# Kernel tuning notes

Hardware: AMD Instinct MI355X
Metric: run time of the kernel (lower is better)

## Reference

```python
import jax, jax.numpy as jnp
import numpy as np

N_STYLE_TOKEN = 10
TOKEN_SIZE = 256   # num_units
NUM_HEADS = 8
D_K = TOKEN_SIZE // NUM_HEADS  # 32, key_dim of cross-attention
D_Q = 256                      # encoder_hidden (add_gst=True, add_positional_encoding=True)
MAX_SEQ_LEN = 2000


def sinusoid_table(n_pos, d):
    pos = np.arange(n_pos, dtype=np.float64)[:, None]
    i = np.arange(d, dtype=np.float64)[None, :]
    angle = pos / np.power(10000.0, 2.0 * (i // 2) / d)
    table = np.zeros((n_pos, d), dtype=np.float64)
    table[:, 0::2] = np.sin(angle[:, 0::2])
    table[:, 1::2] = np.cos(angle[:, 1::2])
    return jnp.asarray(table, dtype=jnp.float32)


def setup_inputs() -> dict:
    key = jax.random.key(0)
    k1, k2, k3, k4, k5, k6 = jax.random.split(key, 6)
    N, T = 64, 2000
    inputs = jax.random.normal(k1, (N, T, D_Q), dtype=jnp.float32)
    positional_indexes = jnp.sort(
        jax.random.randint(k2, (N, T), 0, T), axis=-1).astype(jnp.int64)
    embed = 0.5 * jax.random.normal(k3, (N_STYLE_TOKEN, D_K), dtype=jnp.float32)
    # nn.Linear(in, out, bias=False) weights stored as [out, in]
    Wq = jax.random.normal(k4, (TOKEN_SIZE, D_Q), dtype=jnp.float32) / np.sqrt(D_Q)
    Wk = jax.random.normal(k5, (TOKEN_SIZE, D_K), dtype=jnp.float32) / np.sqrt(D_K)
    Wv = jax.random.normal(k6, (TOKEN_SIZE, D_K), dtype=jnp.float32) / np.sqrt(D_K)
    pos_table = sinusoid_table(MAX_SEQ_LEN + 1, D_Q)  # non-trainable buffer
    return {"inputs": inputs, "positional_indexes": positional_indexes,
            "embed": embed, "Wq": Wq, "Wk": Wk, "Wv": Wv,
            "pos_table": pos_table}


def reference(inputs, positional_indexes, embed, Wq, Wk, Wv, pos_table):
    N, T, dq = inputs.shape
    H, ds = NUM_HEADS, TOKEN_SIZE // NUM_HEADS
    n_tok, d_k = embed.shape

    # per-utterance positional gather (the python for-loop, vectorized):
    # pos_enc_by_scale[i, t] = pos_table[positional_indexes[i, t]]
    pos_enc = pos_table[positional_indexes]            # [N, T, dq]
    x = inputs + pos_enc                               # add_positional_encoding=True

    keys = jnp.tanh(embed)                             # [n_tok, d_k]

    q = jnp.einsum('ntq,uq->ntu', x, Wq)               # [N, T, U]
    k = keys @ Wk.T                                    # [n_tok, U]
    v = keys @ Wv.T                                    # [n_tok, U]

    qh = q.reshape(N, T, H, ds)                        # split heads along units
    kh = k.reshape(n_tok, H, ds)
    vh = v.reshape(n_tok, H, ds)

    logits = jnp.einsum('nthd,khd->nhtk', qh, kh) / jnp.sqrt(
        jnp.asarray(d_k, dtype=qh.dtype))              # [N, H, T, n_tok]
    attn = jax.nn.softmax(logits, axis=-1)

    out = jnp.einsum('nhtk,khd->nthd', attn, vh).reshape(N, T, H * ds)
    # scores: [h,N,T,k] pieces concatenated on last dim, then transpose(1,2)
    scores = jnp.transpose(attn, (0, 1, 3, 2)).reshape(N, H * n_tok, T)
    return out, scores
```

## Files before the change

### kernel.cpp

```cpp
#include <hip/hip_runtime.h>

#define T_SEQ 2000
#define N_UTT 64
#define DQ 256
#define NTOK 10
#define NH 8
#define DS 32

typedef float f32x4 __attribute__((ext_vector_type(4)));
typedef short s16x8 __attribute__((ext_vector_type(8)));

__device__ __forceinline__ unsigned short f2bf(float f){
    unsigned int u = __float_as_uint(f);
    u += 0x7FFFu + ((u >> 16) & 1u);
    return (unsigned short)(u >> 16);
}
__device__ __forceinline__ float bf2f(unsigned short h){
    return __uint_as_float(((unsigned int)h) << 16);
}

__global__ __launch_bounds__(256) void prep_kernel(
    const float* __restrict__ embed, const float* __restrict__ Wq,
    const float* __restrict__ Wk, const float* __restrict__ Wv,
    unsigned short* __restrict__ WqB, float* __restrict__ khd, float* __restrict__ vhd)
{
    const int b = blockIdx.x, t = threadIdx.x;
    if (b < 256){
        const int i = b*256 + t;
        WqB[i] = f2bf(Wq[i]);
    } else {
        for (int tok = 0; tok < NTOK; ++tok){
            float ka = 0.f, va = 0.f;
            #pragma unroll
            for (int d = 0; d < DS; ++d){
                const float kd = tanhf(embed[tok*DS + d]);
                ka += kd * Wk[t*DS + d];
                va += kd * Wv[t*DS + d];
            }
            khd[tok*256 + t] = ka;
            vhd[tok*256 + t] = va;
        }
    }
}

#define XS_STRIDE 264
#define QS_STRIDE 260

__global__ __launch_bounds__(256, 3) void main_kernel(
    const float* __restrict__ inputs, const int* __restrict__ pidx,
    const float* __restrict__ pos_table, const unsigned short* __restrict__ WqB,
    const float* __restrict__ khd, const float* __restrict__ vhd,
    float* __restrict__ outp, float* __restrict__ scores)
{
    __shared__ unsigned short xs_hi[16*XS_STRIDE];
    __shared__ unsigned short xs_lo[16*XS_STRIDE];
    __shared__ float qs[16*QS_STRIDE];
    __shared__ float khL[NTOK*256];
    __shared__ float vhL[NTOK*256];

    const int tid = threadIdx.x;
    const int m0 = blockIdx.x * 16;
    const int n  = m0 / T_SEQ;
    const int t0 = m0 % T_SEQ;

    #pragma unroll
    for (int i = 0; i < NTOK; ++i){
        khL[i*256 + tid] = khd[i*256 + tid];
        vhL[i*256 + tid] = vhd[i*256 + tid];
    }

    {
        const int rsub = tid >> 6;
        const int c    = (tid & 63) * 4;
        #pragma unroll
        for (int p = 0; p < 4; ++p){
            const int r   = p*4 + rsub;
            const int row = m0 + r;
            const int idx = pidx[row];
            const float4 xi = *(const float4*)(inputs    + (size_t)row*DQ + c);
            const float4 pe = *(const float4*)(pos_table + (size_t)idx*DQ + c);
            float xv[4] = {xi.x+pe.x, xi.y+pe.y, xi.z+pe.z, xi.w+pe.w};
            unsigned short hs[4], ls[4];
            #pragma unroll
            for (int j = 0; j < 4; ++j){
                hs[j] = f2bf(xv[j]);
                ls[j] = f2bf(xv[j] - bf2f(hs[j]));
            }
            *(uint2*)&xs_hi[r*XS_STRIDE + c] =
                make_uint2(hs[0] | ((unsigned)hs[1] << 16), hs[2] | ((unsigned)hs[3] << 16));
            *(uint2*)&xs_lo[r*XS_STRIDE + c] =
                make_uint2(ls[0] | ((unsigned)ls[1] << 16), ls[2] | ((unsigned)ls[3] << 16));
        }
    }
    __syncthreads();

    {
        const int wave = tid >> 6;
        const int lane = tid & 63;
        const int lrow = lane & 15;
        const int quad = lane >> 4;
        const int u0w  = wave * 64;

        s16x8 ah[8], al[8];
        #pragma unroll
        for (int kt = 0; kt < 8; ++kt){
            ah[kt] = *(const s16x8*)&xs_hi[lrow*XS_STRIDE + kt*32 + quad*8];
            al[kt] = *(const s16x8*)&xs_lo[lrow*XS_STRIDE + kt*32 + quad*8];
        }
        f32x4 acc[4] = {};
        #pragma unroll
        for (int kt = 0; kt < 8; ++kt){
            s16x8 bfr[4];
            #pragma unroll
            for (int ct = 0; ct < 4; ++ct){
                const int u = u0w + ct*16 + lrow;
                bfr[ct] = *(const s16x8*)(WqB + u*256 + kt*32 + quad*8);
            }
            #pragma unroll
            for (int ct = 0; ct < 4; ++ct){
                acc[ct] = __builtin_amdgcn_mfma_f32_16x16x32_bf16(al[kt], bfr[ct], acc[ct], 0,0,0);
                acc[ct] = __builtin_amdgcn_mfma_f32_16x16x32_bf16(ah[kt], bfr[ct], acc[ct], 0,0,0);
            }
        }
        #pragma unroll
        for (int ct = 0; ct < 4; ++ct){
            #pragma unroll
            for (int reg = 0; reg < 4; ++reg){
                qs[(quad*4 + reg)*QS_STRIDE + u0w + ct*16 + lrow] = acc[ct][reg];
            }
        }
    }
    __syncthreads();

    if (tid < 128){
        const int r = tid & 15;
        const int h = tid >> 4;
        const int t = t0 + r;

        float q[32];
        #pragma unroll
        for (int d = 0; d < 32; d += 4){
            const float4 v4 = *(const float4*)&qs[r*QS_STRIDE + h*32 + d];
            q[d+0]=v4.x; q[d+1]=v4.y; q[d+2]=v4.z; q[d+3]=v4.w;
        }
        const float scale = 0.17677669529663687f;
        float logit[NTOK];
        float mx = -1e30f;
        #pragma unroll
        for (int k = 0; k < NTOK; ++k){
            const float* kp = &khL[k*256 + h*32];
            float a0=0.f,a1=0.f,a2=0.f,a3=0.f;
            #pragma unroll
            for (int d = 0; d < 32; d += 4){
                a0 += q[d+0]*kp[d+0];
                a1 += q[d+1]*kp[d+1];
                a2 += q[d+2]*kp[d+2];
                a3 += q[d+3]*kp[d+3];
            }
            logit[k] = ((a0+a1)+(a2+a3))*scale;
            mx = fmaxf(mx, logit[k]);
        }
        float p[NTOK], s = 0.f;
        #pragma unroll
        for (int k = 0; k < NTOK; ++k){ p[k] = __expf(logit[k]-mx); s += p[k]; }
        const float inv = 1.f/s;
        #pragma unroll
        for (int k = 0; k < NTOK; ++k){
            p[k] *= inv;
            scores[(n*(NH*NTOK) + h*NTOK + k)*T_SEQ + t] = p[k];
        }
        #pragma unroll
        for (int d = 0; d < 32; d += 4){
            float4 o = make_float4(0.f,0.f,0.f,0.f);
            #pragma unroll
            for (int k = 0; k < NTOK; ++k){
                const float4 vv = *(const float4*)&vhL[k*256 + h*32 + d];
                o.x += p[k]*vv.x; o.y += p[k]*vv.y; o.z += p[k]*vv.z; o.w += p[k]*vv.w;
            }
            *(float4*)(outp + (size_t)(m0 + r)*DQ + h*32 + d) = o;
        }
    }
}

extern "C" void kernel_launch(void* const* d_in, const int* in_sizes, int n_in,
                              void* d_out, int out_size, void* d_ws, size_t ws_size,
                              hipStream_t stream)
{
    const float* inputs    = (const float*)d_in[0];
    const int*   pidx      = (const int*)d_in[1];
    const float* embed     = (const float*)d_in[2];
    const float* Wq        = (const float*)d_in[3];
    const float* Wk        = (const float*)d_in[4];
    const float* Wv        = (const float*)d_in[5];
    const float* pos_table = (const float*)d_in[6];

    float* outp   = (float*)d_out;
    float* scores = outp + (size_t)N_UTT*T_SEQ*DQ;

    unsigned short* WqB = (unsigned short*)d_ws;
    float* khd = (float*)((char*)d_ws + 256*256*sizeof(unsigned short));
    float* vhd = khd + NTOK*256;

    prep_kernel<<<257, 256, 0, stream>>>(embed, Wq, Wk, Wv, WqB, khd, vhd);
    main_kernel<<<8000, 256, 0, stream>>>(inputs, pidx, pos_table, WqB, khd, vhd,
                                          outp, scores);
}
```

Before: 460.5 us.

## Fold Wq and key projection into one logit weight matrix

Precomputes a combined 80x256 weight (Wq_h^T * k_h, with the softmax scale folded in) so the main kernel computes logits straight from x with one GEMM instead of projecting to 256-wide q and then taking dot products. The combined weight is split into bf16 hi/lo parts and the product uses three MFMAs for near-fp32 accuracy. The main kernel now runs one wave per 32 rows and loads x directly into registers without staging through LDS. This cuts GEMM width from 256 to 80 columns, at the cost of extra hi/lo MFMAs, an extra prep launch, and uncoalesced per-lane global loads.

```diff
diff --git a/kernel.cpp b/kernel.cpp
--- a/kernel.cpp
+++ b/kernel.cpp
@@ -6,6 +6,8 @@
 #define NTOK 10
 #define NH 8
 #define DS 32
+#define NC 80
+#define LGS 84
 
 typedef float f32x4 __attribute__((ext_vector_type(4)));
 typedef short s16x8 __attribute__((ext_vector_type(8)));
@@ -19,165 +21,148 @@
     return __uint_as_float(((unsigned int)h) << 16);
 }
 
-__global__ __launch_bounds__(256) void prep_kernel(
-    const float* __restrict__ embed, const float* __restrict__ Wq,
-    const float* __restrict__ Wk, const float* __restrict__ Wv,
-    unsigned short* __restrict__ WqB, float* __restrict__ khd, float* __restrict__ vhd)
+__global__ __launch_bounds__(256) void prep_kv(
+    const float* __restrict__ embed, const float* __restrict__ Wk,
+    const float* __restrict__ Wv, float* __restrict__ khd, float* __restrict__ vhd)
 {
-    const int b = blockIdx.x, t = threadIdx.x;
-    if (b < 256){
-        const int i = b*256 + t;
-        WqB[i] = f2bf(Wq[i]);
-    } else {
-        for (int tok = 0; tok < NTOK; ++tok){
-            float ka = 0.f, va = 0.f;
-            #pragma unroll
-            for (int d = 0; d < DS; ++d){
-                const float kd = tanhf(embed[tok*DS + d]);
-                ka += kd * Wk[t*DS + d];
-                va += kd * Wv[t*DS + d];
-            }
-            khd[tok*256 + t] = ka;
-            vhd[tok*256 + t] = va;
+    __shared__ float th[NTOK*DS];
+    const int u = threadIdx.x;
+    for (int i = u; i < NTOK*DS; i += 256) th[i] = tanhf(embed[i]);
+    __syncthreads();
+    for (int tok = 0; tok < NTOK; ++tok){
+        float ka = 0.f, va = 0.f;
+        #pragma unroll
+        for (int d = 0; d < DS; ++d){
+            const float kd = th[tok*DS + d];
+            ka += kd * Wk[u*DS + d];
+            va += kd * Wv[u*DS + d];
         }
+        khd[tok*DQ + u] = ka;
+        vhd[tok*DQ + u] = va;
     }
 }
 
-#define XS_STRIDE 264
-#define QS_STRIDE 260
+__global__ __launch_bounds__(256) void prep_wl(
+    const float* __restrict__ Wq, const float* __restrict__ khd,
+    unsigned short* __restrict__ WlH, unsigned short* __restrict__ WlL)
+{
+    const int c = blockIdx.x;
+    const int q = threadIdx.x;
+    const int h = c / NTOK, tok = c - h*NTOK;
+    float s = 0.f;
+    #pragma unroll
+    for (int d = 0; d < DS; ++d)
+        s += Wq[(size_t)(h*DS + d)*DQ + q] * khd[tok*DQ + h*DS + d];
+    s *= 0.17677669529663687f;
+    const unsigned short hi = f2bf(s);
+    const unsigned short lo = f2bf(s - bf2f(hi));
+    WlH[c*DQ + q] = hi;
+    WlL[c*DQ + q] = lo;
+}
 
-__global__ __launch_bounds__(256, 3) void main_kernel(
+__global__ __launch_bounds__(64, 4) void main_kernel(
     const float* __restrict__ inputs, const int* __restrict__ pidx,
-    const float* __restrict__ pos_table, const unsigned short* __restrict__ WqB,
-    const float* __restrict__ khd, const float* __restrict__ vhd,
+    const float* __restrict__ pos_table, const unsigned short* __restrict__ WlH,
+    const unsigned short* __restrict__ WlL, const float* __restrict__ vhd,
     float* __restrict__ outp, float* __restrict__ scores)
 {
-    __shared__ unsigned short xs_hi[16*XS_STRIDE];
-    __shared__ unsigned short xs_lo[16*XS_STRIDE];
-    __shared__ float qs[16*QS_STRIDE];
-    __shared__ float khL[NTOK*256];
-    __shared__ float vhL[NTOK*256];
+    __shared__ float lg[2][16][LGS];
+    const int lane = threadIdx.x;
+    const int lrow = lane & 15;
+    const int quad = lane >> 4;
+    const int m0   = blockIdx.x * 32;
 
-    const int tid = threadIdx.x;
-    const int m0 = blockIdx.x * 16;
-    const int n  = m0 / T_SEQ;
-    const int t0 = m0 % T_SEQ;
+    const int rowA = m0 + lrow;
+    const int rowB = rowA + 16;
+    const int idxA = pidx[rowA];
+    const int idxB = pidx[rowB];
 
-    #pragma unroll
-    for (int i = 0; i < NTOK; ++i){
-        khL[i*256 + tid] = khd[i*256 + tid];
-        vhL[i*256 + tid] = vhd[i*256 + tid];
-    }
+    f32x4 acc[2][5] = {};
 
-    {
-        const int rsub = tid >> 6;
-        const int c    = (tid & 63) * 4;
+    for (int kt = 0; kt < 8; ++kt){
+        const int kq = kt*32 + quad*8;
+        s16x8 ah[2], al[2];
         #pragma unroll
-        for (int p = 0; p < 4; ++p){
-            const int r   = p*4 + rsub;
-            const int row = m0 + r;
-            const int idx = pidx[row];
-            const float4 xi = *(const float4*)(inputs    + (size_t)row*DQ + c);
-            const float4 pe = *(const float4*)(pos_table + (size_t)idx*DQ + c);
-            float xv[4] = {xi.x+pe.x, xi.y+pe.y, xi.z+pe.z, xi.w+pe.w};
-            unsigned short hs[4], ls[4];
+        for (int mt = 0; mt < 2; ++mt){
+            const float* xp = inputs    + (size_t)(mt ? rowB : rowA)*DQ + kq;
+            const float* pp = pos_table + (size_t)(mt ? idxB : idxA)*DQ + kq;
+            f32x4 x0 = *(const f32x4*)xp;
+            f32x4 x1 = *(const f32x4*)(xp + 4);
+            x0 += *(const f32x4*)pp;
+            x1 += *(const f32x4*)(pp + 4);
+            s16x8 h8, l8;
             #pragma unroll
             for (int j = 0; j < 4; ++j){
-                hs[j] = f2bf(xv[j]);
-                ls[j] = f2bf(xv[j] - bf2f(hs[j]));
+                const unsigned short hv = f2bf(x0[j]);
+                h8[j]   = (short)hv;
+                l8[j]   = (short)f2bf(x0[j] - bf2f(hv));
+                const unsigned short hw = f2bf(x1[j]);
+                h8[4+j] = (short)hw;
+                l8[4+j] = (short)f2bf(x1[j] - bf2f(hw));
             }
-            *(uint2*)&xs_hi[r*XS_STRIDE + c] =
-                make_uint2(hs[0] | ((unsigned)hs[1] << 16), hs[2] | ((unsigned)hs[3] << 16));
-            *(uint2*)&xs_lo[r*XS_STRIDE + c] =
-                make_uint2(ls[0] | ((unsigned)ls[1] << 16), ls[2] | ((unsigned)ls[3] << 16));
-        }
-    }
-    __syncthreads();
-
-    {
-        const int wave = tid >> 6;
-        const int lane = tid & 63;
-        const int lrow = lane & 15;
-        const int quad = lane >> 4;
-        const int u0w  = wave * 64;
-
-        s16x8 ah[8], al[8];
-        #pragma unroll
-        for (int kt = 0; kt < 8; ++kt){
-            ah[kt] = *(const s16x8*)&xs_hi[lrow*XS_STRIDE + kt*32 + quad*8];
-            al[kt] = *(const s16x8*)&xs_lo[lrow*XS_STRIDE + kt*32 + quad*8];
-        }
-        f32x4 acc[4] = {};
-        #pragma unroll
-        for (int kt = 0; kt < 8; ++kt){
-            s16x8 bfr[4];
-            #pragma unroll
-            for (int ct = 0; ct < 4; ++ct){
-                const int u = u0w + ct*16 + lrow;
-                bfr[ct] = *(const s16x8*)(WqB + u*256 + kt*32 + quad*8);
-            }
-            #pragma unroll
-            for (int ct = 0; ct < 4; ++ct){
-                acc[ct] = __builtin_amdgcn_mfma_f32_16x16x32_bf16(al[kt], bfr[ct], acc[ct], 0,0,0);
-                acc[ct] = __builtin_amdgcn_mfma_f32_16x16x32_bf16(ah[kt], bfr[ct], acc[ct], 0,0,0);
-            }
+            ah[mt] = h8; al[mt] = l8;
         }
         #pragma unroll
-        for (int ct = 0; ct < 4; ++ct){
+        for (int ct = 0; ct < 5; ++ct){
+            const s16x8 bh = *(const s16x8*)(WlH + (ct*16 + lrow)*DQ + kq);
+            const s16x8 bl = *(const s16x8*)(WlL + (ct*16 + lrow)*DQ + kq);
             #pragma unroll
-            for (int reg = 0; reg < 4; ++reg){
-                qs[(quad*4 + reg)*QS_STRIDE + u0w + ct*16 + lrow] = acc[ct][reg];
+            for (int mt = 0; mt < 2; ++mt){
+                acc[mt][ct] = __builtin_amdgcn_mfma_f32_16x16x32_bf16(al[mt], bh, acc[mt][ct], 0,0,0);
+                acc[mt][ct] = __builtin_amdgcn_mfma_f32_16x16x32_bf16(ah[mt], bl, acc[mt][ct], 0,0,0);
+                acc[mt][ct] = __builtin_amdgcn_mfma_f32_16x16x32_bf16(ah[mt], bh, acc[mt][ct], 0,0,0);
             }
         }
     }
-    __syncthreads();
 
-    if (tid < 128){
-        const int r = tid & 15;
-        const int h = tid >> 4;
-        const int t = t0 + r;
+    #pragma unroll
+    for (int mt = 0; mt < 2; ++mt)
+        #pragma unroll
+        for (int ct = 0; ct < 5; ++ct)
+            #pragma unroll
+            for (int reg = 0; reg < 4; ++reg)
+                lg[mt][quad*4 + reg][ct*16 + lrow] = acc[mt][ct][reg];
 
-        float q[32];
+    const int r = lrow;
+    #pragma unroll
+    for (int hh = 0; hh < 2; ++hh){
+        const int h = quad + hh*4;
+        float p[2][NTOK];
         #pragma unroll
-        for (int d = 0; d < 32; d += 4){
-            const float4 v4 = *(const float4*)&qs[r*QS_STRIDE + h*32 + d];
-            q[d+0]=v4.x; q[d+1]=v4.y; q[d+2]=v4.z; q[d+3]=v4.w;
-        }
-        const float scale = 0.17677669529663687f;
-        float logit[NTOK];
-        float mx = -1e30f;
-        #pragma unroll
-        for (int k = 0; k < NTOK; ++k){
-            const float* kp = &khL[k*256 + h*32];
-            float a0=0.f,a1=0.f,a2=0.f,a3=0.f;
+        for (int mt = 0; mt < 2; ++mt){
+            float lv[NTOK];
             #pragma unroll
-            for (int d = 0; d < 32; d += 4){
-                a0 += q[d+0]*kp[d+0];
-                a1 += q[d+1]*kp[d+1];
-                a2 += q[d+2]*kp[d+2];
-                a3 += q[d+3]*kp[d+3];
-            }
-            logit[k] = ((a0+a1)+(a2+a3))*scale;
-            mx = fmaxf(mx, logit[k]);
-        }
-        float p[NTOK], s = 0.f;
-        #pragma unroll
-        for (int k = 0; k < NTOK; ++k){ p[k] = __expf(logit[k]-mx); s += p[k]; }
-        const float inv = 1.f/s;
-        #pragma unroll
-        for (int k = 0; k < NTOK; ++k){
-            p[k] *= inv;
-            scores[(n*(NH*NTOK) + h*NTOK + k)*T_SEQ + t] = p[k];
-        }
-        #pragma unroll
-        for (int d = 0; d < 32; d += 4){
-            float4 o = make_float4(0.f,0.f,0.f,0.f);
+            for (int k = 0; k < NTOK; ++k) lv[k] = lg[mt][r][h*NTOK + k];
+            float mx = lv[0];
+            #pragma unroll
+            for (int k = 1; k < NTOK; ++k) mx = fmaxf(mx, lv[k]);
+            float s = 0.f;
+            #pragma unroll
+            for (int k = 0; k < NTOK; ++k){ p[mt][k] = __expf(lv[k] - mx); s += p[mt][k]; }
+            const float inv = 1.f / s;
+            const int row = m0 + mt*16 + r;
+            const int n = row / T_SEQ;
+            const int t = row - n*T_SEQ;
+            float* sp = scores + (size_t)(n*(NH*NTOK) + h*NTOK)*T_SEQ + t;
             #pragma unroll
             for (int k = 0; k < NTOK; ++k){
-                const float4 vv = *(const float4*)&vhL[k*256 + h*32 + d];
-                o.x += p[k]*vv.x; o.y += p[k]*vv.y; o.z += p[k]*vv.z; o.w += p[k]*vv.w;
+                p[mt][k] *= inv;
+                sp[(size_t)k*T_SEQ] = p[mt][k];
             }
-            *(float4*)(outp + (size_t)(m0 + r)*DQ + h*32 + d) = o;
+        }
+        float* o0 = outp + (size_t)(m0 + r)*DQ + h*DS;
+        float* o1 = outp + (size_t)(m0 + 16 + r)*DQ + h*DS;
+        #pragma unroll
+        for (int db = 0; db < 8; ++db){
+            f32x4 a0 = {}, a1 = {};
+            #pragma unroll
+            for (int k = 0; k < NTOK; ++k){
+                const f32x4 vv = *(const f32x4*)(vhd + k*DQ + h*DS + db*4);
+                a0 += p[0][k] * vv;
+                a1 += p[1][k] * vv;
+            }
+            *(f32x4*)(o0 + db*4) = a0;
+            *(f32x4*)(o1 + db*4) = a1;
         }
     }
 }
@@ -197,11 +182,13 @@
     float* outp   = (float*)d_out;
     float* scores = outp + (size_t)N_UTT*T_SEQ*DQ;
 
-    unsigned short* WqB = (unsigned short*)d_ws;
-    float* khd = (float*)((char*)d_ws + 256*256*sizeof(unsigned short));
-    float* vhd = khd + NTOK*256;
+    float* khd = (float*)d_ws;
+    float* vhd = khd + NTOK*DQ;
+    unsigned short* WlH = (unsigned short*)(vhd + NTOK*DQ);
+    unsigned short* WlL = WlH + NC*DQ;
 
-    prep_kernel<<<257, 256, 0, stream>>>(embed, Wq, Wk, Wv, WqB, khd, vhd);
-    main_kernel<<<8000, 256, 0, stream>>>(inputs, pidx, pos_table, WqB, khd, vhd,
-                                          outp, scores);
+    prep_kv<<<1, 256, 0, stream>>>(embed, Wk, Wv, khd, vhd);
+    prep_wl<<<NC, 256, 0, stream>>>(Wq, khd, WlH, WlL);
+    main_kernel<<<(N_UTT*T_SEQ)/32, 64, 0, stream>>>(inputs, pidx, pos_table,
+                                                     WlH, WlL, vhd, outp, scores);
 }
```

Measured after the change: 392.8 us. 1.17x faster.
